# Kernel tuning notes

Measured on AMD Instinct MI355X. Metric: run time of the kernel, lower is better.

## Reference

```python
import jax, jax.numpy as jnp
import numpy as np


def _lstm_layer(x, W, U, b):
    """Keras-style LSTM (gate order i,f,c,o). x: (B,T,F). Returns (hs: (B,T,H), h_last: (B,H))."""
    B, T, F = x.shape
    H = U.shape[0]
    # Precompute input projections for all timesteps: (T, B, 4H)
    zx = jnp.einsum('btf,fk->tbk', x, W) + b

    def step(carry, zx_t):
        h, c = carry
        z = zx_t + h @ U  # (B, 4H)
        i, f, g, o = jnp.split(z, 4, axis=-1)
        i = jax.nn.sigmoid(i)
        f = jax.nn.sigmoid(f)
        g = jnp.tanh(g)
        o = jax.nn.sigmoid(o)
        c = f * c + i * g
        h = o * jnp.tanh(c)
        return (h, c), h

    h0 = jnp.zeros((B, H), dtype=x.dtype)
    c0 = jnp.zeros((B, H), dtype=x.dtype)
    (h_last, _), hs = jax.lax.scan(step, (h0, c0), zx)
    return jnp.transpose(hs, (1, 0, 2)), h_last


def setup_inputs() -> dict:
    key = jax.random.key(0)
    ks = jax.random.split(key, 8)
    B, T, F, H, L = 512, 128, 64, 1024, 1
    s = 0.05
    return {
        'x': jax.random.normal(ks[0], (B, T, F), dtype=jnp.float32),
        'W1': jax.random.normal(ks[1], (F, 4 * H), dtype=jnp.float32) * s,
        'U1': jax.random.normal(ks[2], (H, 4 * H), dtype=jnp.float32) * s,
        'b1': jnp.zeros((4 * H,), dtype=jnp.float32),
        'W2': jax.random.normal(ks[3], (H, 4 * H), dtype=jnp.float32) * s,
        'U2': jax.random.normal(ks[4], (H, 4 * H), dtype=jnp.float32) * s,
        'b2': jnp.zeros((4 * H,), dtype=jnp.float32),
        'Wd': jax.random.normal(ks[5], (H, L), dtype=jnp.float32) * s,
        'bd': jnp.zeros((L,), dtype=jnp.float32),
    }


def reference(x, W1, U1, b1, W2, U2, b2, Wd, bd):
    # Layer 1: return_sequences=True (dropout inactive at inference)
    h1_seq, _ = _lstm_layer(x, W1, U1, b1)
    # Layer 2: return_sequences=False -> last hidden state
    _, h2_last = _lstm_layer(h1_seq, W2, U2, b2)
    # Dense sigmoid head
    return jax.nn.sigmoid(h2_last @ Wd + bd)
```

## Files before the change

kernel.cpp:

```cpp
#include <hip/hip_runtime.h>
#include <hip/hip_bf16.h>
#include <cstdint>


typedef __attribute__((ext_vector_type(8))) _Float16 half8;
typedef __attribute__((ext_vector_type(4))) float    float4v;

__device__ __forceinline__ float sigf(float x) { return 1.0f / (1.0f + __expf(-x)); }
__device__ __forceinline__ float tanhfast(float x) { return 2.0f * sigf(2.0f * x) - 1.0f; }

static constexpr size_t HPS = 32ull * 32 * 512;

struct FragSet {
    half8 A[4];
    half8 B[4][2];
};

__global__ __launch_bounds__(256, 1) void fused_step(
    int s,
    const _Float16* __restrict__ xp,
    const _Float16* __restrict__ P1,
    const _Float16* __restrict__ P2,
    const float* __restrict__ b1, float* __restrict__ c1, _Float16* __restrict__ h1p,
    const float* __restrict__ b2, float* __restrict__ c2, _Float16* __restrict__ h2p)
{
    const int b    = blockIdx.x;
    const int role = (b >> 3) & 1;
    const int tile = ((b >> 4) << 3) | (b & 7);

    const _Float16 *As0, *As1, *Pk;
    const float* bias; float* cs; _Float16* hop;
    int KC0, KCB, KCT;
    if (role == 0) {
        const int t = s; if (t >= 128) return;
        As0 = xp + (size_t)t * 32768;  KC0 = 2;
        As1 = h1p + (size_t)(t & 1) * HPS;
        Pk = P1; KCB = 34; KCT = 34;
        bias = b1; cs = c1;
        hop = h1p + (size_t)(1 - (t & 1)) * HPS;
    } else {
        const int t = s - 1; if (t < 0) return;
        As0 = h1p + (size_t)(1 - (t & 1)) * HPS; KC0 = 32;
        As1 = h2p + (size_t)(t & 1) * HPS;
        Pk = P2; KCB = 64; KCT = 64;
        bias = b2; cs = c2;
        hop = h2p + (size_t)(1 - (t & 1)) * HPS;
    }

    const int tid = threadIdx.x;
    const int w   = tid >> 6;
    const int l   = tid & 63;
    const int q   = l >> 4;
    const int c16 = l & 15;
    const int mh  = w & 1;
    const int kp  = w >> 1;

    const int m0  = (tile >> 5) * 128;
    const int n0  = (tile & 31) * 32;
    const int mG0 = (m0 >> 4) + mh * 4;

    const size_t l8 = (size_t)l * 8;

    const _Float16* bp[4][2];
#pragma unroll
    for (int g = 0; g < 4; ++g)
#pragma unroll
        for (int nf = 0; nf < 2; ++nf)
            bp[g][nf] = Pk + ((size_t)(g * 64 + (n0 >> 4) + nf) * KCB) * 512 + l8;

    float4v acc[4][4][2] = {};

    auto loadS = [&](int kc, FragSet& S) {
        const _Float16* ab; size_t astr;
        if (kc < KC0) { ab = As0 + (size_t)kc * 512;         astr = (size_t)KC0 * 512; }
        else          { ab = As1 + (size_t)(kc - KC0) * 512; astr = 32ull * 512; }
        ab += (size_t)mG0 * astr + l8;
#pragma unroll
        for (int ms = 0; ms < 4; ++ms)
            S.A[ms] = *(const half8*)(ab + (size_t)ms * astr);
#pragma unroll
        for (int g = 0; g < 4; ++g)
#pragma unroll
            for (int nf = 0; nf < 2; ++nf)
                S.B[g][nf] = *(const half8*)(bp[g][nf] + (size_t)kc * 512);
    };
    auto computeS = [&](const FragSet& S) {
#pragma unroll
        for (int g = 0; g < 4; ++g)
#pragma unroll
            for (int ms = 0; ms < 4; ++ms)
#pragma unroll
                for (int nf = 0; nf < 2; ++nf)
                    acc[g][ms][nf] = __builtin_amdgcn_mfma_f32_16x16x32_f16(
                        S.A[ms], S.B[g][nf], acc[g][ms][nf], 0, 0, 0);
    };

    const int KCH = KCT >> 1;
    const int kcS = kp ? KCH : 0;
    const int kcE = kp ? KCT : KCH;

    FragSet S0, S1;
    loadS(kcS, S0);
    int kc = kcS;
    for (; kc + 2 <= kcE; kc += 2) {
        loadS(kc + 1, S1);
        computeS(S0);
        if (kc + 2 < kcE) loadS(kc + 2, S0);
        computeS(S1);
    }
    if (kc < kcE) computeS(S0);

    __shared__ float4v red[4][16][64];
    if (kp == 0) {
#pragma unroll
        for (int g = 0; g < 4; ++g)
#pragma unroll
            for (int ms = 0; ms < 4; ++ms)
                red[w][g * 4 + ms][l] = acc[g][ms][1];
    } else {
#pragma unroll
        for (int g = 0; g < 4; ++g)
#pragma unroll
            for (int ms = 0; ms < 4; ++ms)
                red[w][g * 4 + ms][l] = acc[g][ms][0];
    }
    __syncthreads();
    float4v out[4][4];
    if (kp == 0) {
#pragma unroll
        for (int g = 0; g < 4; ++g)
#pragma unroll
            for (int ms = 0; ms < 4; ++ms)
                out[g][ms] = acc[g][ms][0] + red[w ^ 2][g * 4 + ms][l];
    } else {
#pragma unroll
        for (int g = 0; g < 4; ++g)
#pragma unroll
            for (int ms = 0; ms < 4; ++ms)
                out[g][ms] = acc[g][ms][1] + red[w ^ 2][g * 4 + ms][l];
    }

    const int ng = n0 + kp * 16 + c16;
    const float bi  = bias[ng];
    const float bff = bias[1024 + ng];
    const float bg  = bias[2048 + ng];
    const float bo  = bias[3072 + ng];
    const int kcH   = n0 >> 5;
    const int laneW = (kp * 2 + (c16 >> 3)) << 4;
    const int jW    = c16 & 7;
#pragma unroll
    for (int ms = 0; ms < 4; ++ms) {
        const int mG = mG0 + ms;
        _Float16* hg = hop + ((size_t)(mG * 32 + kcH)) * 512 + (size_t)laneW * 8 + jW;
#pragma unroll
        for (int i = 0; i < 4; ++i) {
            const int m = m0 + mh * 64 + ms * 16 + q * 4 + i;
            const float zi = out[0][ms][i] + bi;
            const float zf = out[1][ms][i] + bff;
            const float zg = out[2][ms][i] + bg;
            const float zo = out[3][ms][i] + bo;
            const float ig = sigf(zi);
            const float fg = sigf(zf);
            const float gg = tanhfast(zg);
            const float og = sigf(zo);
            const size_t cidx = (size_t)m * 1024 + ng;
            const float cc = fg * cs[cidx] + ig * gg;
            cs[cidx] = cc;
            hg[(q * 4 + i) * 8] = (_Float16)(og * tanhfast(cc));
        }
    }
}

__global__ void pack_weights(const float* __restrict__ W, const float* __restrict__ U,
                             int KA, int KC, _Float16* __restrict__ out)
{
    const size_t e = (size_t)blockIdx.x * blockDim.x + threadIdx.x;
    const size_t total = (size_t)256 * KC * 512;
    if (e >= total) return;
    const int j    = (int)(e & 7);
    const int lane = (int)((e >> 3) & 63);
    const size_t g = e >> 9;
    const int kc  = (int)(g % KC);
    const int ntG = (int)(g / KC);
    const int col = ntG * 16 + (lane & 15);
    const int k   = kc * 32 + (lane >> 4) * 8 + j;
    const float v = (k < KA) ? W[(size_t)k * 4096 + col]
                             : U[(size_t)(k - KA) * 4096 + col];
    out[e] = (_Float16)v;
}

__global__ void pack_x(const float* __restrict__ x, _Float16* __restrict__ xp)
{
    const int e = blockIdx.x * blockDim.x + threadIdx.x;
    if (e >= 512 * 128 * 64) return;
    const int j  = e & 7;
    const int l  = (e >> 3) & 63;
    const int g  = e >> 9;
    const int kc = g & 1;
    const int tm = g >> 1;
    const int mG = tm & 31;
    const int t  = tm >> 5;
    const int m  = mG * 16 + (l & 15);
    const int f  = kc * 32 + (l >> 4) * 8 + j;
    xp[e] = (_Float16)x[((size_t)m * 128 + t) * 64 + f];
}

__global__ __launch_bounds__(64) void dense_head(const _Float16* __restrict__ h2p,
                                                 const float* __restrict__ Wd,
                                                 const float* __restrict__ bd,
                                                 float* __restrict__ out)
{
    const int mG = blockIdx.x;
    const int l  = threadIdx.x;
    float s = 0.0f;
    for (int kc = 0; kc < 32; ++kc) {
        half8 f = *(const half8*)(h2p + ((size_t)(mG * 32 + kc)) * 512 + (size_t)l * 8);
        const int kb = kc * 32 + (l >> 4) * 8;
#pragma unroll
        for (int j = 0; j < 8; ++j) s += (float)f[j] * Wd[kb + j];
    }
    s += __shfl_xor(s, 16);
    s += __shfl_xor(s, 32);
    if (l < 16) out[mG * 16 + l] = 1.0f / (1.0f + __expf(-(s + bd[0])));
}


extern "C" void kernel_launch(void* const* d_in, const int* in_sizes, int n_in,
                              void* d_out, int out_size, void* d_ws, size_t ws_size,
                              hipStream_t stream)
{
    const float* x  = (const float*)d_in[0];
    const float* W1 = (const float*)d_in[1];
    const float* U1 = (const float*)d_in[2];
    const float* b1 = (const float*)d_in[3];
    const float* W2 = (const float*)d_in[4];
    const float* U2 = (const float*)d_in[5];
    const float* b2 = (const float*)d_in[6];
    const float* Wd = (const float*)d_in[7];
    const float* bd = (const float*)d_in[8];
    float* out = (float*)d_out;

    char* ws = (char*)d_ws;
    size_t off = 0;
    auto alloc = [&](size_t bytes) {
        char* p = ws + off;
        off = (off + bytes + 255) & ~(size_t)255;
        return p;
    };
    _Float16* xp  = (_Float16*)alloc(512ull * 128 * 64 * 2);
    _Float16* P1  = (_Float16*)alloc(256ull * 34 * 512 * 2);
    _Float16* P2  = (_Float16*)alloc(256ull * 64 * 512 * 2);
    _Float16* h1p = (_Float16*)alloc(2ull * HPS * 2);
    _Float16* h2p = (_Float16*)alloc(2ull * HPS * 2);
    float*    c1  = (float*)alloc(512ull * 1024 * 4);
    float*    c2  = (float*)alloc(512ull * 1024 * 4);

    hipMemsetAsync(c1, 0, 512ull * 1024 * 4, stream);
    hipMemsetAsync(c2, 0, 512ull * 1024 * 4, stream);
    hipMemsetAsync(h1p, 0, HPS * 2, stream);
    hipMemsetAsync(h2p, 0, HPS * 2, stream);

    pack_x<<<(512 * 128 * 64 + 255) / 256, 256, 0, stream>>>(x, xp);
    pack_weights<<<(256 * 34 * 512 + 255) / 256, 256, 0, stream>>>(W1, U1, 64, 34, P1);
    pack_weights<<<(256 * 64 * 512 + 255) / 256, 256, 0, stream>>>(W2, U2, 1024, 64, P2);

    for (int s = 0; s <= 128; ++s) {
        fused_step<<<256, 256, 0, stream>>>(s, xp, P1, P2,
                                            b1, c1, h1p, b2, c2, h2p);
    }
    dense_head<<<32, 64, 0, stream>>>(h2p, Wd, bd, out);
}
```

Before: 3.186 ms.

## Split K across four waves per tile with two-stage LDS reduction

Doubles the block to 512 threads so each output tile's K range is split four ways instead of two. Partial sums are combined with a two-level shared-memory reduction, and each wave then applies the gate math to half the rows. The aim is to shorten the serial per-step K loop and raise wave count on this latency-bound recurrent step. In exchange it adds two more barriers, doubles the LDS reduction buffer, drops the explicit double-buffered prefetch, and tighter launch bounds may force register spills.

```diff
diff --git a/kernel.cpp b/kernel.cpp
--- a/kernel.cpp
+++ b/kernel.cpp
@@ -16,7 +16,7 @@
     half8 B[4][2];
 };
 
-__global__ __launch_bounds__(256, 1) void fused_step(
+__global__ __launch_bounds__(512, 2) void fused_step(
     int s,
     const _Float16* __restrict__ xp,
     const _Float16* __restrict__ P1,
@@ -95,23 +95,20 @@
                         S.A[ms], S.B[g][nf], acc[g][ms][nf], 0, 0, 0);
     };
 
-    const int KCH = KCT >> 1;
-    const int kcS = kp ? KCH : 0;
-    const int kcE = kp ? KCT : KCH;
-
-    FragSet S0, S1;
-    loadS(kcS, S0);
-    int kc = kcS;
-    for (; kc + 2 <= kcE; kc += 2) {
-        loadS(kc + 1, S1);
-        computeS(S0);
-        if (kc + 2 < kcE) loadS(kc + 2, S0);
-        computeS(S1);
-    }
-    if (kc < kcE) computeS(S0);
-
-    __shared__ float4v red[4][16][64];
-    if (kp == 0) {
+    const int base = KCT >> 2;
+    const int rem  = KCT & 3;
+    const int len  = base + (kp < rem ? 1 : 0);
+    const int kcS  = kp * base + (kp < rem ? kp : rem);
+
+    FragSet S;
+#pragma unroll 2
+    for (int kc = kcS; kc < kcS + len; ++kc) {
+        loadS(kc, S);
+        computeS(S);
+    }
+
+    __shared__ float4v red[8][16][64];
+    if ((kp & 1) == 0) {
 #pragma unroll
         for (int g = 0; g < 4; ++g)
 #pragma unroll
@@ -125,40 +122,72 @@
                 red[w][g * 4 + ms][l] = acc[g][ms][0];
     }
     __syncthreads();
-    float4v out[4][4];
-    if (kp == 0) {
-#pragma unroll
-        for (int g = 0; g < 4; ++g)
-#pragma unroll
-            for (int ms = 0; ms < 4; ++ms)
-                out[g][ms] = acc[g][ms][0] + red[w ^ 2][g * 4 + ms][l];
-    } else {
-#pragma unroll
-        for (int g = 0; g < 4; ++g)
-#pragma unroll
-            for (int ms = 0; ms < 4; ++ms)
-                out[g][ms] = acc[g][ms][1] + red[w ^ 2][g * 4 + ms][l];
-    }
-
-    const int ng = n0 + kp * 16 + c16;
+    float4v acc1[4][4];
+    if ((kp & 1) == 0) {
+#pragma unroll
+        for (int g = 0; g < 4; ++g)
+#pragma unroll
+            for (int ms = 0; ms < 4; ++ms)
+                acc1[g][ms] = acc[g][ms][0] + red[w ^ 2][g * 4 + ms][l];
+    } else {
+#pragma unroll
+        for (int g = 0; g < 4; ++g)
+#pragma unroll
+            for (int ms = 0; ms < 4; ++ms)
+                acc1[g][ms] = acc[g][ms][1] + red[w ^ 2][g * 4 + ms][l];
+    }
+    __syncthreads();
+    if ((kp >> 1) == 0) {
+#pragma unroll
+        for (int g = 0; g < 4; ++g)
+#pragma unroll
+            for (int j = 0; j < 2; ++j)
+                red[w][g * 2 + j][l] = acc1[g][2 + j];
+    } else {
+#pragma unroll
+        for (int g = 0; g < 4; ++g)
+#pragma unroll
+            for (int j = 0; j < 2; ++j)
+                red[w][g * 2 + j][l] = acc1[g][j];
+    }
+    __syncthreads();
+    float4v out[4][2];
+    if ((kp >> 1) == 0) {
+#pragma unroll
+        for (int g = 0; g < 4; ++g)
+#pragma unroll
+            for (int j = 0; j < 2; ++j)
+                out[g][j] = acc1[g][j] + red[w ^ 4][g * 2 + j][l];
+    } else {
+#pragma unroll
+        for (int g = 0; g < 4; ++g)
+#pragma unroll
+            for (int j = 0; j < 2; ++j)
+                out[g][j] = acc1[g][2 + j] + red[w ^ 4][g * 2 + j][l];
+    }
+
+    const int own_nf  = kp & 1;
+    const int own_msp = kp >> 1;
+    const int ng = n0 + own_nf * 16 + c16;
     const float bi  = bias[ng];
     const float bff = bias[1024 + ng];
     const float bg  = bias[2048 + ng];
     const float bo  = bias[3072 + ng];
     const int kcH   = n0 >> 5;
-    const int laneW = (kp * 2 + (c16 >> 3)) << 4;
+    const int laneW = (own_nf * 2 + (c16 >> 3)) << 4;
     const int jW    = c16 & 7;
 #pragma unroll
-    for (int ms = 0; ms < 4; ++ms) {
-        const int mG = mG0 + ms;
+    for (int j = 0; j < 2; ++j) {
+        const int msg = own_msp * 2 + j;
+        const int mG  = mG0 + msg;
         _Float16* hg = hop + ((size_t)(mG * 32 + kcH)) * 512 + (size_t)laneW * 8 + jW;
 #pragma unroll
         for (int i = 0; i < 4; ++i) {
-            const int m = m0 + mh * 64 + ms * 16 + q * 4 + i;
-            const float zi = out[0][ms][i] + bi;
-            const float zf = out[1][ms][i] + bff;
-            const float zg = out[2][ms][i] + bg;
-            const float zo = out[3][ms][i] + bo;
+            const int m = m0 + mh * 64 + msg * 16 + q * 4 + i;
+            const float zi = out[0][j][i] + bi;
+            const float zf = out[1][j][i] + bff;
+            const float zg = out[2][j][i] + bg;
+            const float zo = out[3][j][i] + bo;
             const float ig = sigf(zi);
             const float fg = sigf(zf);
             const float gg = tanhfast(zg);
@@ -265,7 +294,7 @@
     pack_weights<<<(256 * 64 * 512 + 255) / 256, 256, 0, stream>>>(W2, U2, 1024, 64, P2);
 
     for (int s = 0; s <= 128; ++s) {
-        fused_step<<<256, 256, 0, stream>>>(s, xp, P1, P2,
+        fused_step<<<256, 512, 0, stream>>>(s, xp, P1, P2,
                                             b1, c1, h1p, b2, c2, h2p);
     }
     dense_head<<<32, 64, 0, stream>>>(h2p, Wd, bd, out);
```

Result: faster. 3.034 ms (-4.8%).
